# Kernel tuning notes

Measured on AMD Instinct MI355X. Metric: run time of the kernel, lower is better.

Reference implementation:

```python
import jax, jax.numpy as jnp
import numpy as np

N = 9
CELLS = N * N  # 81
B = 1024
HID = 100
EMPTY_P = 0.3


def _build_constraint_mask():
    # (81, 3, 81): mask[q, g, k] = 1 if cell k is in the same row/col/box as cell q
    m = np.zeros((CELLS, 3, CELLS), np.float32)
    for q in range(CELLS):
        r, c = divmod(q, N)
        for k in range(CELLS):
            r2, c2 = divmod(k, N)
            if r2 == r:
                m[q, 0, k] = 1.0
            if c2 == c:
                m[q, 1, k] = 1.0
            if (r2 // 3 == r // 3) and (c2 // 3 == c // 3):
                m[q, 2, k] = 1.0
    return jnp.asarray(m)


def setup_inputs() -> dict:
    key = jax.random.key(0)
    k1, k2, k3, k4 = jax.random.split(key, 4)
    # partially-filled boards: one-hot digits, ~EMPTY_P of cells zeroed (empty)
    digits = jax.random.randint(k1, (B, CELLS), 0, N)
    onehot = jax.nn.one_hot(digits, N, dtype=jnp.float32)
    filled = (jax.random.uniform(k2, (B, CELLS)) > EMPTY_P).astype(jnp.float32)
    x = onehot * filled[..., None]
    W1 = jax.random.normal(k3, (HID, 3 * N), dtype=jnp.float32) * 0.1
    W2 = jax.random.normal(k4, (N, HID), dtype=jnp.float32) * 0.1
    c = _build_constraint_mask()
    return {"x": x, "c": c, "W1": W1, "W2": W2}


def reference(x, c, W1, W2):
    bts = x.shape[0]
    # min_empty: max number of empty cells over the batch (fixed loop count, as in torch)
    T = int(jnp.max(jnp.sum(x.sum(axis=2) == 0, axis=1)))
    bidx = jnp.arange(bts)

    def step(carry, _):
        xc, xp = carry
        # constraints[b,q,g,d] = sum_k xc[b,k,d] * c[q,g,k]  (sparse graph aggregation)
        cons = jnp.einsum('bkd,qgk->bqgd', xc, c).reshape(bts, CELLS, 3 * N)
        empty = xc.sum(axis=2) == 0  # (B, 81)
        # masked MLP: compute everywhere, use only where empty (same math)
        y = jax.nn.relu(cons @ W1.T) @ W2.T  # (B, 81, 9)
        s_ = jax.nn.softmax(y, axis=-1)
        xp = jnp.where(empty[..., None], s_, xp)
        s = jnp.where(empty[..., None], s_, 0.0)
        score = s.max(axis=2)           # (B, 81)
        score_pos = s.argmax(axis=2)    # (B, 81)
        mmax = score.argmax(axis=1)     # (B,) most confident empty cell per board
        digit = score_pos[bidx, mmax]   # (B,)
        new_x = xc.at[bidx, mmax, digit].set(1.0)
        has_empty = empty.any(axis=1)
        xc = jnp.where(has_empty[:, None, None], new_x, xc)
        return (xc, xp), None

    (x_final, x_pred), _ = jax.lax.scan(step, (x, x), None, length=T)
    return (x_pred, x_final)
```

## Files before the change

### kernel.cpp

```cpp
#include <hip/hip_runtime.h>

#define CELLS 81
#define ND 9
#define HID 100
#define NP 52
#define PPW 13

typedef float v2f __attribute__((ext_vector_type(2)));

#define W1P_SZ (9 * NP * 8)
#define W2P_SZ (NP * 20)
#define NE_OFF (W1P_SZ + W2P_SZ)
#define ORD_OFF (NE_OFF + 1024)

__global__ __launch_bounds__(64) void prep_kernel(
    const float* __restrict__ W1, const float* __restrict__ W2,
    float* __restrict__ ws)
{
    const int t = threadIdx.x;
    for (int i = t; i < 9 * NP; i += 64) {
        int d = i / NP, j = i - d * NP;
        float* r = ws + (size_t)i * 8;
        if (j < 50) {
            int u0 = 2 * j, u1 = u0 + 1;
            r[0] = W1[u0*27 + d];      r[1] = W1[u1*27 + d];
            r[2] = W1[u0*27 + 9 + d];  r[3] = W1[u1*27 + 9 + d];
            r[4] = W1[u0*27 + 18 + d]; r[5] = W1[u1*27 + 18 + d];
        } else {
            r[0]=r[1]=r[2]=r[3]=r[4]=r[5]=0.f;
        }
        r[6] = 0.f; r[7] = 0.f;
    }
    for (int j = t; j < NP; j += 64) {
        float* r = ws + W1P_SZ + (size_t)j * 20;
        if (j < 50) {
            int u0 = 2 * j, u1 = u0 + 1;
            #pragma unroll
            for (int d = 0; d < ND; ++d) {
                r[2*d]     = W2[d*HID + u0];
                r[2*d + 1] = W2[d*HID + u1];
            }
        } else {
            #pragma unroll
            for (int d = 0; d < ND; ++d) { r[2*d] = 0.f; r[2*d+1] = 0.f; }
        }
        r[18] = 0.f; r[19] = 0.f;
    }
}

__global__ __launch_bounds__(64) void ne_kernel(
    const float* __restrict__ x_all, int* __restrict__ ne, int nBoards)
{
    const int b = blockIdx.x, t = threadIdx.x;
    const float* xb = x_all + (size_t)b * (CELLS * ND);
    float mx = 0.f;
    #pragma unroll
    for (int d = 0; d < ND; ++d) mx = fmaxf(mx, xb[t*ND + d]);
    bool e1 = (mx < 0.5f);
    bool e2 = false;
    if (t < CELLS - 64) {
        float m2 = 0.f;
        #pragma unroll
        for (int d = 0; d < ND; ++d) m2 = fmaxf(m2, xb[(64+t)*ND + d]);
        e2 = (m2 < 0.5f);
    }
    unsigned long long m1 = __ballot(e1), m2b = __ballot(e2);
    if (t == 0) ne[b] = __popcll(m1) + __popcll(m2b);
}

__global__ __launch_bounds__(1024) void part_kernel(
    const int* __restrict__ ne, int* __restrict__ order, int nBoards)
{
    __shared__ int sc[1024];
    const int t = threadIdx.x;
    const bool valid = t < nBoards;
    int isS = valid ? ((ne[t] <= 32) ? 1 : 0) : 0;
    sc[t] = isS;
    __syncthreads();
    for (int off = 1; off < 1024; off <<= 1) {
        int v = (t >= off) ? sc[t - off] : 0;
        __syncthreads();
        sc[t] += v;
        __syncthreads();
    }
    const int nSmall = sc[1023];
    const int excl = sc[t] - isS;
    for (int i = t; i < 2048; i += 1024) order[i] = -1;
    __syncthreads();
    const int nPair = (nSmall + 1) >> 1;
    if (valid) {
        if (isS) order[excl] = t;
        else {
            int k = t - excl;
            int base = 2 * nPair + 2 * k;
            order[base] = t; order[base + 1] = t;
        }
    }
    __syncthreads();
    if (t == 0 && (nSmall & 1)) order[nSmall] = order[nSmall - 1];
}

__global__ __launch_bounds__(256, 4) void sudoku_kernel(
    const float* __restrict__ x_all,
    const float* __restrict__ ws,
    const int* __restrict__ order,
    float* __restrict__ out, int nBoards)
{
    const int tid = threadIdx.x;
    const int wv  = tid >> 6;
    const int lw  = tid & 63;
    const int h   = lw >> 5;
    const int jbase = wv * PPW;

    const int s0  = order[2 * blockIdx.x];
    const int s1r = order[2 * blockIdx.x + 1];
    if (s0 < 0) return;
    const int s1 = (s1r < 0) ? s0 : s1r;
    const bool joined = (s0 == s1);
    const int myBoard = h ? s1 : s0;
    const int idx = joined ? 0 : h;

    float* pom = out + (size_t)myBoard * (CELLS * ND);

    __shared__ __align__(16) float w1s[W1P_SZ];
    __shared__ __align__(16) float w2s[W2P_SZ];
    __shared__ float parts[2][4][ND][64];
    __shared__ float cnt[2][3 * 81];
    __shared__ int   digit[2][CELLS];

    for (int i = tid; i < W1P_SZ / 4; i += 256)
        ((float4*)w1s)[i] = ((const float4*)ws)[i];
    for (int i = tid; i < W2P_SZ / 4; i += 256)
        ((float4*)w2s)[i] = ((const float4*)(ws + W1P_SZ))[i];
    for (int i = tid; i < 2 * 243; i += 256) (&cnt[0][0])[i] = 0.f;
    __syncthreads();

    {
        const int slot = (tid < 128) ? 0 : 1;
        const int t = (tid < 128) ? tid : tid - 128;
        const bool doSlot = (slot == 0) || !joined;
        const int bd = slot ? s1 : s0;
        const float* xb = x_all + (size_t)bd * (CELLS * ND);
        float* pob = out + (size_t)bd * (CELLS * ND);
        if (doSlot) {
            if (t < CELLS) {
                int dig = -1;
                #pragma unroll
                for (int d = 0; d < ND; ++d)
                    if (dig < 0 && xb[t*ND + d] > 0.5f) dig = d;
                digit[slot][t] = dig;
                if (dig >= 0) {
                    int r = t/9, c = t%9, b = (r/3)*3 + c/3;
                    atomicAdd(&cnt[slot][r*9 + dig], 1.f);
                    atomicAdd(&cnt[slot][81 + c*9 + dig], 1.f);
                    atomicAdd(&cnt[slot][162 + b*9 + dig], 1.f);
                }
            }
            for (int i = t; i < CELLS * ND; i += 128) pob[i] = xb[i];
        }
    }
    __syncthreads();

    const int rank = joined ? lw : (lw & 31);
    int myq = 127;
    int ne0 = 0, ne1 = 0;
    for (int q = 0; q < CELLS; ++q)
        if (digit[0][q] < 0) { if (idx == 0 && ne0 == rank) myq = q; ++ne0; }
    if (!joined) {
        for (int q = 0; q < CELLS; ++q)
            if (digit[1][q] < 0) { if (idx == 1 && ne1 == rank) myq = q; ++ne1; }
    } else ne1 = ne0;
    const int ne_mine = idx ? ne1 : ne0;
    const int itMax = max(ne0, ne1);
    bool active = (rank < ne_mine);

    const int myr = (myq < 81) ? myq / 9 : 0;
    const int myc = (myq < 81) ? myq % 9 : 0;
    const int myb = (myr / 3) * 3 + myc / 3;

    float crr[9], ccc[9], cbb[9];
    #pragma unroll
    for (int j = 0; j < 9; ++j) {
        crr[j] = cnt[idx][myr*9 + j];
        ccc[j] = cnt[idx][81 + myc*9 + j];
        cbb[j] = cnt[idx][162 + myb*9 + j];
    }
    v2f z2[PPW];
    #pragma unroll
    for (int j = 0; j < PPW; ++j) {
        v2f a = (v2f){0.f, 0.f};
        #pragma unroll
        for (int d = 0; d < 9; ++d) {
            const float* p = &w1s[(d*NP + jbase + j) * 8];
            float4 ab = *(const float4*)p;
            v2f Cv = *(const v2f*)(p + 4);
            v2f Av = (v2f){ab.x, ab.y}, Bv = (v2f){ab.z, ab.w};
            a += crr[d]*Av + ccc[d]*Bv + cbb[d]*Cv;
        }
        z2[j] = a;
    }

    int dc = 0;
    v2f b0v = (v2f){0.f,0.f}, b1v = (v2f){0.f,0.f}, b2v = (v2f){0.f,0.f};
    float pfin[ND];

    for (int it = 0; it < itMax; ++it) {
        const float* w1r = &w1s[(dc*NP + jbase) * 8];
        const float* w2r = &w2s[jbase * 20];

        v2f acc2[ND];
        #pragma unroll
        for (int d = 0; d < ND; ++d) acc2[d] = (v2f){0.f, 0.f};

        #pragma unroll
        for (int j = 0; j < PPW; ++j) {
            const float* p = w1r + j*8;
            float4 ab = *(const float4*)p;
            v2f Cv = *(const v2f*)(p + 4);
            v2f Av = (v2f){ab.x, ab.y}, Bv = (v2f){ab.z, ab.w};
            v2f zv = z2[j];
            zv = b0v*Av + (b1v*Bv + (b2v*Cv + zv));
            z2[j] = zv;
            v2f hh;
            hh.x = fmaxf(zv.x, 0.f);
            hh.y = fmaxf(zv.y, 0.f);
            const float* qq = w2r + j*20;
            float4 w01 = *(const float4*)qq;
            float4 w23 = *(const float4*)(qq + 4);
            float4 w45 = *(const float4*)(qq + 8);
            float4 w67 = *(const float4*)(qq + 12);
            v2f w8 = *(const v2f*)(qq + 16);
            acc2[0] += hh * (v2f){w01.x, w01.y};
            acc2[1] += hh * (v2f){w01.z, w01.w};
            acc2[2] += hh * (v2f){w23.x, w23.y};
            acc2[3] += hh * (v2f){w23.z, w23.w};
            acc2[4] += hh * (v2f){w45.x, w45.y};
            acc2[5] += hh * (v2f){w45.z, w45.w};
            acc2[6] += hh * (v2f){w67.x, w67.y};
            acc2[7] += hh * (v2f){w67.z, w67.w};
            acc2[8] += hh * w8;
        }

        const int buf = it & 1;
        #pragma unroll
        for (int d = 0; d < ND; ++d)
            parts[buf][wv][d][lw] = acc2[d].x + acc2[d].y;
        __syncthreads();

        float acc[ND];
        #pragma unroll
        for (int d = 0; d < ND; ++d) acc[d] = parts[buf][0][d][lw];
        #pragma unroll
        for (int ow = 1; ow < 4; ++ow) {
            #pragma unroll
            for (int d = 0; d < ND; ++d) acc[d] += parts[buf][ow][d][lw];
        }

        float m9 = fmaxf(fmaxf(fmaxf(acc[0],acc[1]), fmaxf(acc[2],acc[3])),
                         fmaxf(fmaxf(acc[4],acc[5]), fmaxf(acc[6],acc[7])));
        m9 = fmaxf(m9, acc[8]);
        float s = 0.f;
        #pragma unroll
        for (int d = 0; d < ND; ++d) { acc[d] = __expf(acc[d] - m9); s += acc[d]; }
        float inv = 1.f / s;
        float bv = -1.f; int bd = 0;
        #pragma unroll
        for (int d = 0; d < ND; ++d) {
            acc[d] *= inv;
            if (acc[d] > bv) { bv = acc[d]; bd = d; }
        }

        float bvv = active ? bv : -1.f;
        float vmax = bvv;
        #pragma unroll
        for (int off = 16; off >= 1; off >>= 1)
            vmax = fmaxf(vmax, __shfl_xor(vmax, off));
        if (joined) vmax = fmaxf(vmax, __shfl_xor(vmax, 32));
        const unsigned long long segMask =
            joined ? ~0ull : (h ? 0xFFFFFFFF00000000ull : 0x00000000FFFFFFFFull);
        unsigned long long msk = __ballot(active && (bvv == vmax)) & segMask;
        const bool valid = (msk != 0);
        int wl = valid ? (__ffsll(msk) - 1) : 0;
        int qw = __shfl(myq, wl);
        int dwn = __shfl(bd, wl);

        if (active && valid && myq == qw) {
            #pragma unroll
            for (int d = 0; d < ND; ++d) pfin[d] = acc[d];
            if (wv == 0) digit[idx][myq] = dwn;
            active = false;
        }
        const int pr = qw/9, pcc = qw%9, pb = (pr/3)*3 + pcc/3;
        b0v = (v2f)((valid && myr == pr)  ? 1.f : 0.f);
        b1v = (v2f)((valid && myc == pcc) ? 1.f : 0.f);
        b2v = (v2f)((valid && myb == pb)  ? 1.f : 0.f);
        if (valid) dc = dwn;
    }

    __syncthreads();
    if (wv == 0 && myq < 81) {
        #pragma unroll
        for (int d = 0; d < ND; ++d) pom[myq*ND + d] = pfin[d];
    }
    {
        const int slot = (tid < 128) ? 0 : 1;
        const int t = (tid < 128) ? tid : tid - 128;
        const bool doSlot = (slot == 0) || !joined;
        const int bd2 = slot ? s1 : s0;
        float* fob = out + (size_t)nBoards * (CELLS * ND) + (size_t)bd2 * (CELLS * ND);
        if (doSlot) {
            for (int i = t; i < CELLS * ND; i += 128) {
                int q = i / ND, d = i - q * ND;
                fob[i] = (digit[slot][q] == d) ? 1.f : 0.f;
            }
        }
    }
}

extern "C" void kernel_launch(void* const* d_in, const int* in_sizes, int n_in,
                              void* d_out, int out_size, void* d_ws, size_t ws_size,
                              hipStream_t stream) {
    const float* x  = (const float*)d_in[0];
    const float* W1 = (const float*)d_in[2];
    const float* W2 = (const float*)d_in[3];
    float* out = (float*)d_out;
    float* ws  = (float*)d_ws;
    int nBoards = in_sizes[0] / (CELLS * ND);
    int* neArr  = (int*)ws + NE_OFF;
    int* ordArr = (int*)ws + ORD_OFF;
    prep_kernel<<<1, 64, 0, stream>>>(W1, W2, ws);
    ne_kernel<<<nBoards, 64, 0, stream>>>(x, neArr, nBoards);
    part_kernel<<<1, 1024, 0, stream>>>(neArr, ordArr, nBoards);
    sudoku_kernel<<<nBoards, 256, 0, stream>>>(x, ws, ordArr, out, nBoards);
}
```

Before: 139.6 us.

## Cache part of W2 in registers and sort boards by empty count

The main kernel now preloads W2 weights for the first 8 hidden pairs of each wave into registers, which cuts LDS reads in the inner loop. Launch bounds drop from 4 to 2 blocks per SM to leave room for the extra registers. The partition kernel swaps its prefix-scan split for a full descending sort by empty-cell count, so boards paired into one block have similar iteration counts. The empty-cell counts are also clamped to 64. The costs are lower occupancy and a quadratic-time sort.

```diff
diff --git a/kernel.cpp b/kernel.cpp
--- a/kernel.cpp
+++ b/kernel.cpp
@@ -5,6 +5,7 @@
 #define HID 100
 #define NP 52
 #define PPW 13
+#define NREG 8
 
 typedef float v2f __attribute__((ext_vector_type(2)));
 
@@ -71,36 +72,34 @@
 __global__ __launch_bounds__(1024) void part_kernel(
     const int* __restrict__ ne, int* __restrict__ order, int nBoards)
 {
-    __shared__ int sc[1024];
+    __shared__ int s_ne[1024];
+    __shared__ int s_nBig;
     const int t = threadIdx.x;
-    const bool valid = t < nBoards;
-    int isS = valid ? ((ne[t] <= 32) ? 1 : 0) : 0;
-    sc[t] = isS;
-    __syncthreads();
-    for (int off = 1; off < 1024; off <<= 1) {
-        int v = (t >= off) ? sc[t - off] : 0;
-        __syncthreads();
-        sc[t] += v;
-        __syncthreads();
-    }
-    const int nSmall = sc[1023];
-    const int excl = sc[t] - isS;
+    s_ne[t] = (t < nBoards) ? ne[t] : -1;
+    if (t == 0) s_nBig = 0;
     for (int i = t; i < 2048; i += 1024) order[i] = -1;
     __syncthreads();
-    const int nPair = (nSmall + 1) >> 1;
-    if (valid) {
-        if (isS) order[excl] = t;
-        else {
-            int k = t - excl;
-            int base = 2 * nPair + 2 * k;
-            order[base] = t; order[base + 1] = t;
-        }
-    }
-    __syncthreads();
-    if (t == 0 && (nSmall & 1)) order[nSmall] = order[nSmall - 1];
-}
-
-__global__ __launch_bounds__(256, 4) void sudoku_kernel(
+    const int key = s_ne[t];
+    int pos = 0;
+    for (int j = 0; j < 1024; ++j) {
+        int kj = s_ne[j];
+        pos += (kj > key) || (kj == key && j < t);
+    }
+    if (t < nBoards && key > 32) atomicAdd(&s_nBig, 1);
+    __syncthreads();
+    const int nBig = s_nBig;
+    if (t < nBoards) {
+        if (pos < nBig) {
+            order[2*pos] = t; order[2*pos + 1] = t;
+        } else {
+            int r = pos - nBig;
+            int b = nBig + (r >> 1);
+            order[2*b + (r & 1)] = t;
+        }
+    }
+}
+
+__global__ __launch_bounds__(256, 2) void sudoku_kernel(
     const float* __restrict__ x_all,
     const float* __restrict__ ws,
     const int* __restrict__ order,
@@ -134,6 +133,14 @@
         ((float4*)w2s)[i] = ((const float4*)(ws + W1P_SZ))[i];
     for (int i = tid; i < 2 * 243; i += 256) (&cnt[0][0])[i] = 0.f;
     __syncthreads();
+
+    float w2reg[NREG][18];
+    #pragma unroll
+    for (int j = 0; j < NREG; ++j) {
+        const float* qq = &w2s[(jbase + j) * 20];
+        #pragma unroll
+        for (int k = 0; k < 18; ++k) w2reg[j][k] = qq[k];
+    }
 
     {
         const int slot = (tid < 128) ? 0 : 1;
@@ -170,6 +177,8 @@
         for (int q = 0; q < CELLS; ++q)
             if (digit[1][q] < 0) { if (idx == 1 && ne1 == rank) myq = q; ++ne1; }
     } else ne1 = ne0;
+    if (ne0 > 64) ne0 = 64;
+    if (ne1 > 64) ne1 = 64;
     const int ne_mine = idx ? ne1 : ne0;
     const int itMax = max(ne0, ne1);
     bool active = (rank < ne_mine);
@@ -224,21 +233,27 @@
             v2f hh;
             hh.x = fmaxf(zv.x, 0.f);
             hh.y = fmaxf(zv.y, 0.f);
-            const float* qq = w2r + j*20;
-            float4 w01 = *(const float4*)qq;
-            float4 w23 = *(const float4*)(qq + 4);
-            float4 w45 = *(const float4*)(qq + 8);
-            float4 w67 = *(const float4*)(qq + 12);
-            v2f w8 = *(const v2f*)(qq + 16);
-            acc2[0] += hh * (v2f){w01.x, w01.y};
-            acc2[1] += hh * (v2f){w01.z, w01.w};
-            acc2[2] += hh * (v2f){w23.x, w23.y};
-            acc2[3] += hh * (v2f){w23.z, w23.w};
-            acc2[4] += hh * (v2f){w45.x, w45.y};
-            acc2[5] += hh * (v2f){w45.z, w45.w};
-            acc2[6] += hh * (v2f){w67.x, w67.y};
-            acc2[7] += hh * (v2f){w67.z, w67.w};
-            acc2[8] += hh * w8;
+            if (j < NREG) {
+                #pragma unroll
+                for (int d = 0; d < ND; ++d)
+                    acc2[d] += hh * (v2f){w2reg[j][2*d], w2reg[j][2*d + 1]};
+            } else {
+                const float* qq = w2r + j*20;
+                float4 w01 = *(const float4*)qq;
+                float4 w23 = *(const float4*)(qq + 4);
+                float4 w45 = *(const float4*)(qq + 8);
+                float4 w67 = *(const float4*)(qq + 12);
+                v2f w8 = *(const v2f*)(qq + 16);
+                acc2[0] += hh * (v2f){w01.x, w01.y};
+                acc2[1] += hh * (v2f){w01.z, w01.w};
+                acc2[2] += hh * (v2f){w23.x, w23.y};
+                acc2[3] += hh * (v2f){w23.z, w23.w};
+                acc2[4] += hh * (v2f){w45.x, w45.y};
+                acc2[5] += hh * (v2f){w45.z, w45.w};
+                acc2[6] += hh * (v2f){w67.x, w67.y};
+                acc2[7] += hh * (v2f){w67.z, w67.w};
+                acc2[8] += hh * w8;
+            }
         }
 
         const int buf = it & 1;
```

Measured after the change: 149.8 us. +7.3%, slower.
